# Performance work log

Measured on AMD Instinct MI355X. Metric: run time of the kernel, lower is better.

## Reference

```python
import jax, jax.numpy as jnp
import numpy as np

N = 50000      # num_nodes
E = 800000     # num_edges (avg degree 16)
IC, OC = 2, 2  # in_channels, out_channels
DIN, DOUT = 128, 128
K = 3          # number of hops


def setup_inputs() -> dict:
    key = jax.random.key(0)
    k1, k2, k3, k4 = jax.random.split(key, 4)
    x = jax.random.normal(k1, (IC, N, DIN), dtype=jnp.float32)
    edge_index = jax.random.randint(k2, (2, E), 0, N, dtype=jnp.int32)
    a = np.sqrt(6.0 / (DIN + DOUT)).astype(np.float32)  # xavier_uniform bound
    W = jax.random.uniform(k3, (OC, IC, DIN, DOUT), minval=-a, maxval=a, dtype=jnp.float32)
    params = jax.random.uniform(k4, (OC, IC, K + 1), minval=0.0, maxval=0.01, dtype=jnp.float32)
    return {"x": x, "edge_index": edge_index, "W": W, "params": params}


def reference(x, edge_index, W, params):
    # x: [IC, N, DIN]; edge_index: [2, E]; W: [OC, IC, DIN, DOUT]; params: [OC, IC, K+1]
    n = x.shape[1]
    k_hops = params.shape[-1] - 1
    row, col = edge_index[0], edge_index[1]

    # normalize_adj: symmetric D^-1/2 A D^-1/2 on unit-valued edges
    deg = jax.ops.segment_sum(jnp.ones(row.shape[0], x.dtype), row, num_segments=n)
    dinv = jnp.where(deg > 0, jax.lax.rsqrt(deg), jnp.zeros_like(deg))
    val = dinv[row] * dinv[col]  # [E]

    def spmm(X):  # A_norm @ X per channel; X: [IC, N, d]
        gathered = X[:, col, :] * val[None, :, None]  # [IC, E, d]
        return jax.vmap(lambda g: jax.ops.segment_sum(g, row, num_segments=n))(gathered)

    # Hop features: H[m] = A^m x, computed once (hoisting the redundant spmm in the torch loop)
    hops = [x]
    for _ in range(k_hops):
        hops.append(spmm(hops[-1]))
    H = jnp.stack(hops)  # [K+1, IC, N, DIN]

    # out[i] = sum_j sum_m params[i,j,m] * (A^m x_j) @ W[i,j]
    return jnp.einsum('mjnd,ijm,ijdf->inf', H, params, W)  # [OC, N, DOUT]
```

## Files before the change

### kernel.cpp

```cpp
#include <hip/hip_runtime.h>
#include <hip/hip_bf16.h>
#include <stdint.h>

#define NN 50000
#define NE 800000
#define D 128
#define KH 3
#define SCAN_B ((NN + 255) / 256)
#define SLOTS 48
#define XB 6250
#define SCB8 391
#define WBB 1024

typedef __attribute__((ext_vector_type(8))) __bf16 bf16x8;
typedef __attribute__((ext_vector_type(4))) float f32x4;
typedef uint32_t u32x2 __attribute__((ext_vector_type(2)));

__device__ __forceinline__ uint16_t bf16_rne(float f) {
  uint32_t u = __builtin_bit_cast(uint32_t, f);
  u = (u + 0x7fffu + ((u >> 16) & 1u)) >> 16;
  return (uint16_t)u;
}
__device__ __forceinline__ uint32_t bf16_pack(float lo, float hi) {
  return ((uint32_t)bf16_rne(hi) << 16) | (uint32_t)bf16_rne(lo);
}

#define GLDS16(gp, lp)                                                         \
  __builtin_amdgcn_global_load_lds(                                            \
      (__attribute__((address_space(1))) void*)(gp),                           \
      (__attribute__((address_space(3))) void*)(lp), 16, 0, 0)

__global__ void k_build3(const int* __restrict__ ei, const float* __restrict__ x,
                         const float* __restrict__ W, const float* __restrict__ params,
                         int* __restrict__ cnt, uint16_t* __restrict__ slots,
                         uint16_t* __restrict__ hop0g, uint16_t* __restrict__ wb) {
  int b = blockIdx.x, t = threadIdx.x;
  if (b < SCB8) {
    int e0 = b * 2048 + t;
    int r8[8], c8[8], p8[8];
#pragma unroll
    for (int u = 0; u < 8; ++u) {
      int e = e0 + u * 256;
      bool ok = e < NE;
      r8[u] = ok ? ei[e] : 0;
      c8[u] = ok ? ei[e + NE] : 0;
    }
#pragma unroll
    for (int u = 0; u < 8; ++u) {
      int e = e0 + u * 256;
      p8[u] = (e < NE) ? atomicAdd(&cnt[r8[u]], 1) : SLOTS;
    }
#pragma unroll
    for (int u = 0; u < 8; ++u)
      if (p8[u] < SLOTS) slots[r8[u] * SLOTS + p8[u]] = (uint16_t)c8[u];
  } else if (b < SCB8 + XB) {
    int base = ((b - SCB8) * 256 + t) * 8;
    int n = base >> 8, c0 = base & 255;
    int j = c0 >> 7, dd = c0 & 127;
    const float* xp = x + (size_t)j * NN * D + (size_t)n * D + dd;
    float4 f0 = *(const float4*)xp;
    float4 f1 = *(const float4*)(xp + 4);
    uint4 o;
    o.x = bf16_pack(f0.x, f0.y);
    o.y = bf16_pack(f0.z, f0.w);
    o.z = bf16_pack(f1.x, f1.y);
    o.w = bf16_pack(f1.z, f1.w);
    *(uint4*)(hop0g + base) = o;
  } else {
    int idx = (b - SCB8 - XB) * 256 + t;
    int c = idx >> 10, k = idx & 1023;
    int i = c >> 7, f = c & 127, m = k >> 8, j = (k >> 7) & 1, dd = k & 127;
    float p = params[(i * 2 + j) * 4 + m];
    float w = W[((i * 2 + j) * 128 + dd) * 128 + f];
    wb[idx] = bf16_rne(p * w);
  }
}

template <int P1>
__global__ void k_spmmu4(const int* __restrict__ cnt, float* __restrict__ dinvw,
                         const uint16_t* __restrict__ slots,
                         const uint16_t* __restrict__ src, uint16_t* __restrict__ dst) {
  const int lane = threadIdx.x & 63;
  const int wid = threadIdx.x >> 6;
  const int r = blockIdx.x * 4 + wid;
  if (r >= NN) return;
  const int dg = __builtin_amdgcn_readfirstlane(cnt[r]);
  const int dgc = dg < SLOTS ? dg : SLOTS;
  const int s = r * SLOTS;
  const int e = s + dgc;
  const int lo = lane * 4;

  float a0 = 0.f, a1 = 0.f, a2 = 0.f, a3 = 0.f;
  for (int i = s; i < e; i += 8) {
    int cw[8];
    float vw[8];
    u32x2 g[8];
#pragma unroll
    for (int u = 0; u < 8; ++u) {
      int idx = i + u;
      bool ok = idx < e;
      cw[u] = (int)slots[ok ? idx : e - 1];
      float vv;
      if (P1) {
        int dc = cnt[cw[u]];
        vv = (dc > 0) ? rsqrtf((float)dc) : 0.0f;
      } else {
        vv = dinvw[cw[u]];
      }
      vw[u] = ok ? vv : 0.0f;
    }
#pragma unroll
    for (int u = 0; u < 8; ++u)
      g[u] = *(const u32x2*)(src + (size_t)cw[u] * 256 + lo);
#pragma unroll
    for (int u = 0; u < 8; ++u) {
      float v = vw[u];
      a0 = fmaf(v, __builtin_bit_cast(float, g[u][0] << 16), a0);
      a1 = fmaf(v, __builtin_bit_cast(float, g[u][0] & 0xffff0000u), a1);
      a2 = fmaf(v, __builtin_bit_cast(float, g[u][1] << 16), a2);
      a3 = fmaf(v, __builtin_bit_cast(float, g[u][1] & 0xffff0000u), a3);
    }
  }
  float sc = (dg > 0) ? rsqrtf((float)dg) : 0.0f;
  if (P1 && lane == 0) dinvw[r] = sc;
  u32x2 o;
  o[0] = bf16_pack(a0 * sc, a1 * sc);
  o[1] = bf16_pack(a2 * sc, a3 * sc);
  *(u32x2*)(dst + (size_t)r * 256 + lo) = o;
}

__global__ __launch_bounds__(256) void k_gemm2(
    const uint16_t* __restrict__ h0, const uint16_t* __restrict__ h1,
    const uint16_t* __restrict__ h2, const uint16_t* __restrict__ h3,
    const uint16_t* __restrict__ wb, float* __restrict__ out) {
  __shared__ __align__(16) uint16_t As[64 * 64];
  __shared__ __align__(16) uint16_t Bs[256 * 64];
  const uint16_t* hops[4] = {h0, h1, h2, h3};
  int t = threadIdx.x;
  int lane = t & 63, wid = t >> 6;
  int wn = wid;
  int m0 = blockIdx.x * 64;
  int rl = lane & 15, q = lane >> 4;
  f32x4 acc[4][4] = {};
#pragma unroll
  for (int hop = 0; hop < 4; ++hop) {
    const uint16_t* hm = hops[hop];
#pragma unroll
    for (int kin = 0; kin < 256; kin += 64) {
      int k0 = hop * 256 + kin;
      {
#pragma unroll
        for (int rr = 0; rr < 2; ++rr) {
          int c = rr * 256 + t;
          int row = c >> 3, kcL = c & 7;
          int kcG = kcL ^ (row & 7);
          int gr = m0 + row;
          gr = gr < NN ? gr : NN - 1;
          GLDS16(hm + (size_t)gr * 256 + kin + kcG * 8, &As[c * 8]);
        }
      }
      {
#pragma unroll
        for (int rr = 0; rr < 8; ++rr) {
          int c = rr * 256 + t;
          int cc = c >> 3, kcL = c & 7;
          int kcG = kcL ^ (cc & 7);
          GLDS16(wb + (size_t)cc * 1024 + k0 + kcG * 8, &Bs[c * 8]);
        }
      }
      __syncthreads();
#pragma unroll
      for (int kq2 = 0; kq2 < 2; ++kq2) {
        int w = kq2 * 4 + q;
        bf16x8 af[4], bq[4];
#pragma unroll
        for (int f = 0; f < 4; ++f) {
          int row = f * 16 + rl;
          af[f] = *(const bf16x8*)(&As[row * 64 + (w ^ (row & 7)) * 8]);
          int col = wn * 64 + f * 16 + rl;
          bq[f] = *(const bf16x8*)(&Bs[col * 64 + (w ^ (col & 7)) * 8]);
        }
#pragma unroll
        for (int fm = 0; fm < 4; ++fm)
#pragma unroll
          for (int fn = 0; fn < 4; ++fn)
            acc[fm][fn] = __builtin_amdgcn_mfma_f32_16x16x32_bf16(af[fm], bq[fn],
                                                                  acc[fm][fn], 0, 0, 0);
      }
      __syncthreads();
    }
  }
#pragma unroll
  for (int fm = 0; fm < 4; ++fm) {
#pragma unroll
    for (int r = 0; r < 4; ++r) {
      int rowg = m0 + fm * 16 + q * 4 + r;
      if (rowg >= NN) continue;
#pragma unroll
      for (int fn = 0; fn < 4; ++fn) {
        int col = wn * 64 + fn * 16 + rl;
        int iOut = col >> 7, colg = col & 127;
        out[((size_t)iOut * NN + rowg) * D + colg] = acc[fm][fn][r];
      }
    }
  }
}

__global__ void k_deg(const int* __restrict__ row, int* __restrict__ deg) {
  int e = blockIdx.x * 256 + threadIdx.x;
  if (e < NE) atomicAdd(&deg[row[e]], 1);
}

__global__ void k_dinv_bsum(const int* __restrict__ deg, float* __restrict__ dinv,
                            int* __restrict__ bsum) {
  __shared__ int s[256];
  int t = threadIdx.x;
  int i = blockIdx.x * 256 + t;
  int d = (i < NN) ? deg[i] : 0;
  if (i < NN) dinv[i] = (d > 0) ? rsqrtf((float)d) : 0.0f;
  s[t] = d;
  __syncthreads();
  for (int off = 128; off > 0; off >>= 1) {
    if (t < off) s[t] += s[t + off];
    __syncthreads();
  }
  if (t == 0) bsum[blockIdx.x] = s[0];
}

__global__ void k_rpwrite(const int* __restrict__ deg, const int* __restrict__ bsum,
                          int* __restrict__ rp, int* __restrict__ cur) {
  __shared__ int s[256];
  __shared__ int sboff;
  int t = threadIdx.x;
  int b = blockIdx.x;
  int pv = (t < b) ? bsum[t] : 0;
  s[t] = pv;
  __syncthreads();
  for (int off = 128; off > 0; off >>= 1) {
    if (t < off) s[t] += s[t + off];
    __syncthreads();
  }
  if (t == 0) sboff = s[0];
  __syncthreads();
  int i = b * 256 + t;
  int v = (i < NN) ? deg[i] : 0;
  s[t] = v;
  __syncthreads();
  for (int off = 1; off < 256; off <<= 1) {
    int u = (t >= off) ? s[t - off] : 0;
    __syncthreads();
    s[t] += u;
    __syncthreads();
  }
  if (i < NN) {
    int r = sboff + s[t] - v;
    rp[i] = r;
    cur[i] = r;
  }
  if (i == 0) rp[NN] = NE;
}

__global__ void k_scatter(const int* __restrict__ row, const int* __restrict__ col,
                          const float* __restrict__ dinv, int* __restrict__ cur,
                          int2* __restrict__ csr) {
  int e = blockIdx.x * 256 + threadIdx.x;
  if (e < NE) {
    int r = row[e], c = col[e];
    int pos = atomicAdd(&cur[r], 1);
    csr[pos] = make_int2(c, __float_as_int(dinv[r] * dinv[c]));
  }
}

__global__ void k_wbig_f(const float* __restrict__ W, const float* __restrict__ params,
                         uint16_t* __restrict__ wb) {
  int idx = blockIdx.x * 256 + threadIdx.x;
  if (idx >= 2 * 256 * 512) return;
  int j = idx >> 17, c = (idx >> 9) & 255, k = idx & 511;
  int i = c >> 7, f = c & 127, m = k >> 7, dd = k & 127;
  float p = params[(i * 2 + j) * 4 + m];
  float w = W[((i * 2 + j) * 128 + dd) * 128 + f];
  wb[idx] = bf16_rne(p * w);
}

__global__ void k_x2h_f(const float* __restrict__ xj, uint16_t* __restrict__ dst) {
  int idx = blockIdx.x * 256 + threadIdx.x;
  if (idx < NN * D) dst[idx] = bf16_rne(xj[idx]);
}

template <int NCH>
__global__ void k_spmm(const int* __restrict__ rp, const int2* __restrict__ csr,
                       const uint16_t* __restrict__ src, uint16_t* __restrict__ dst) {
  constexpr int STRIDE = NCH * 128;
  typedef uint32_t gvec __attribute__((ext_vector_type(NCH)));
  const int lane = threadIdx.x & 63;
  const int wid = threadIdx.x >> 6;
  const int r = blockIdx.x * 4 + wid;
  if (r >= NN) return;
  const int s = __builtin_amdgcn_readfirstlane(rp[r]);
  const int e = __builtin_amdgcn_readfirstlane(rp[r + 1]);
  const int lo = lane * 2 * NCH;

  float a[2 * NCH] = {};
  for (int i = s; i < e; i += 8) {
    int2 cv[8];
    gvec g[8];
#pragma unroll
    for (int u = 0; u < 8; ++u) {
      int idx = i + u;
      bool ok = idx < e;
      cv[u] = csr[ok ? idx : e - 1];
      if (!ok) cv[u].y = 0;
    }
#pragma unroll
    for (int u = 0; u < 8; ++u)
      g[u] = *(const gvec*)(src + (size_t)cv[u].x * STRIDE + lo);
#pragma unroll
    for (int u = 0; u < 8; ++u) {
      float v = __int_as_float(cv[u].y);
#pragma unroll
      for (int q = 0; q < NCH; ++q) {
        a[2 * q] = fmaf(v, __builtin_bit_cast(float, g[u][q] << 16), a[2 * q]);
        a[2 * q + 1] =
            fmaf(v, __builtin_bit_cast(float, g[u][q] & 0xffff0000u), a[2 * q + 1]);
      }
    }
  }
  gvec o;
#pragma unroll
  for (int q = 0; q < NCH; ++q) o[q] = bf16_pack(a[2 * q], a[2 * q + 1]);
  *(gvec*)(dst + (size_t)r * STRIDE + lo) = o;
}

template <int KTOT, int HOPW, int ACCUM>
__global__ __launch_bounds__(256) void k_gemm(
    const uint16_t* __restrict__ h0, const uint16_t* __restrict__ h1,
    const uint16_t* __restrict__ h2, const uint16_t* __restrict__ h3,
    const uint16_t* __restrict__ wb, float* __restrict__ out) {
  __shared__ __align__(16) uint16_t As[128 * 64];
  __shared__ __align__(16) uint16_t Bs[128 * 64];
  const uint16_t* hops[4] = {h0, h1, h2, h3};
  int t = threadIdx.x;
  int lane = t & 63, wid = t >> 6;
  int wm = wid >> 1, wn = wid & 1;
  int m0 = blockIdx.x * 128;
  int c0 = blockIdx.y * 128;
  int rl = lane & 15, q = lane >> 4;
  f32x4 acc[4][4] = {};
#pragma unroll
  for (int hop = 0; hop < KTOT / HOPW; ++hop) {
    const uint16_t* hm = hops[hop];
#pragma unroll
    for (int kin = 0; kin < HOPW; kin += 64) {
      int k0 = hop * HOPW + kin;
#pragma unroll
      for (int rr = 0; rr < 4; ++rr) {
        int c = rr * 256 + t;
        int row = c >> 3, kcL = c & 7;
        int kcG = kcL ^ (row & 7);
        int gr = m0 + row;
        gr = gr < NN ? gr : NN - 1;
        GLDS16(hm + (size_t)gr * HOPW + kin + kcG * 8, &As[c * 8]);
      }
#pragma unroll
      for (int rr = 0; rr < 4; ++rr) {
        int c = rr * 256 + t;
        int cc = c >> 3, kcL = c & 7;
        int kcG = kcL ^ (cc & 7);
        GLDS16(wb + (size_t)(c0 + cc) * KTOT + k0 + kcG * 8, &Bs[c * 8]);
      }
      __syncthreads();
#pragma unroll
      for (int kq2 = 0; kq2 < 2; ++kq2) {
        int w = kq2 * 4 + q;
        bf16x8 af[4], bq[4];
#pragma unroll
        for (int f = 0; f < 4; ++f) {
          int row = wm * 64 + f * 16 + rl;
          af[f] = *(const bf16x8*)(&As[row * 64 + (w ^ (row & 7)) * 8]);
          int col = wn * 64 + f * 16 + rl;
          bq[f] = *(const bf16x8*)(&Bs[col * 64 + (w ^ (col & 7)) * 8]);
        }
#pragma unroll
        for (int fm = 0; fm < 4; ++fm)
#pragma unroll
          for (int fn = 0; fn < 4; ++fn)
            acc[fm][fn] = __builtin_amdgcn_mfma_f32_16x16x32_bf16(af[fm], bq[fn],
                                                                  acc[fm][fn], 0, 0, 0);
      }
      __syncthreads();
    }
  }
  int iOut = blockIdx.y;
#pragma unroll
  for (int fm = 0; fm < 4; ++fm) {
#pragma unroll
    for (int r = 0; r < 4; ++r) {
      int rowg = m0 + wm * 64 + fm * 16 + q * 4 + r;
      if (rowg >= NN) continue;
      float* op = out + ((size_t)iOut * NN + rowg) * D;
#pragma unroll
      for (int fn = 0; fn < 4; ++fn) {
        int colg = wn * 64 + fn * 16 + rl;
        if (ACCUM)
          op[colg] += acc[fm][fn][r];
        else
          op[colg] = acc[fm][fn][r];
      }
    }
  }
}

extern "C" void kernel_launch(void* const* d_in, const int* in_sizes, int n_in,
                              void* d_out, int out_size, void* d_ws, size_t ws_size,
                              hipStream_t stream) {
  (void)in_sizes; (void)n_in; (void)out_size;
  const float* x = (const float*)d_in[0];
  const int* ei = (const int*)d_in[1];
  const float* W = (const float*)d_in[2];
  const float* params = (const float*)d_in[3];
  float* out = (float*)d_out;
  char* ws = (char*)d_ws;

  size_t off = 0;
  auto take = [&](size_t bytes) {
    char* p = ws + off;
    off = (off + bytes + 255) & ~(size_t)255;
    return p;
  };

  int* cnt = (int*)take((size_t)NN * 4);
  float* dinvw = (float*)take((size_t)NN * 4);
  uint16_t* slots = (uint16_t*)take((size_t)NN * SLOTS * 2);
  uint16_t* wb = (uint16_t*)take((size_t)256 * 1024 * 2);
  size_t hopC = (size_t)NN * 256 * 2;
  size_t needC = off + 4 * hopC + 1024;

  if (ws_size >= needC) {
    uint16_t* hop0g = (uint16_t*)take(hopC);
    uint16_t* h1 = (uint16_t*)take(hopC);
    uint16_t* h2 = (uint16_t*)take(hopC);
    uint16_t* h3 = (uint16_t*)take(hopC);
    (void)hipMemsetAsync(cnt, 0, (size_t)NN * 4, stream);
    k_build3<<<SCB8 + XB + WBB, 256, 0, stream>>>(ei, x, W, params, cnt, slots,
                                                  hop0g, wb);
    k_spmmu4<1><<<(NN + 3) / 4, 256, 0, stream>>>(cnt, dinvw, slots, hop0g, h1);
    k_spmmu4<0><<<(NN + 3) / 4, 256, 0, stream>>>(cnt, dinvw, slots, h1, h2);
    k_spmmu4<0><<<(NN + 3) / 4, 256, 0, stream>>>(cnt, dinvw, slots, h2, h3);
    k_gemm2<<<(NN + 63) / 64, 256, 0, stream>>>(hop0g, h1, h2, h3, wb, out);
  } else {
    off = 0;
    int* deg = (int*)take((size_t)NN * 4);
    float* dinv = (float*)take((size_t)NN * 4);
    int* rp = (int*)take((size_t)(NN + 1) * 4);
    int* cur = (int*)take((size_t)NN * 4);
    int* bsum = (int*)take(256 * 4);
    int2* csr = (int2*)take((size_t)NE * 8);
    uint16_t* wbf = (uint16_t*)take((size_t)256 * 1024 * 2);
    (void)hipMemsetAsync(deg, 0, (size_t)NN * 4, stream);
    k_deg<<<(NE + 255) / 256, 256, 0, stream>>>(ei, deg);
    k_dinv_bsum<<<SCAN_B, 256, 0, stream>>>(deg, dinv, bsum);
    k_rpwrite<<<SCAN_B, 256, 0, stream>>>(deg, bsum, rp, cur);
    k_scatter<<<(NE + 255) / 256, 256, 0, stream>>>(ei, ei + NE, dinv, cur, csr);
    size_t hopF = (size_t)NN * 128 * 2;
    uint16_t* hop[4];
    for (int m = 0; m < 4; ++m) hop[m] = (uint16_t*)take(hopF);
    k_wbig_f<<<(2 * 256 * 512 + 255) / 256, 256, 0, stream>>>(W, params, wbf);
    for (int j = 0; j < 2; ++j) {
      k_x2h_f<<<(NN * D + 255) / 256, 256, 0, stream>>>(x + (size_t)j * NN * D, hop[0]);
      for (int m = 1; m <= KH; ++m)
        k_spmm<1><<<(NN + 3) / 4, 256, 0, stream>>>(rp, csr, hop[m - 1], hop[m]);
      dim3 grid((NN + 127) / 128, 2);
      if (j == 0)
        k_gemm<512, 128, 0><<<grid, 256, 0, stream>>>(hop[0], hop[1], hop[2], hop[3],
                                                      wbf, out);
      else
        k_gemm<512, 128, 1><<<grid, 256, 0, stream>>>(hop[0], hop[1], hop[2], hop[3],
                                                      wbf + 256 * 512, out);
    }
  }
}
```

Measured before the change: 347.9 us.

## Fuse build and three SpMM passes into one cooperative persistent kernel

```diff
diff --git a/kernel.cpp b/kernel.cpp
--- a/kernel.cpp
+++ b/kernel.cpp
@@ -1,4 +1,5 @@
 #include <hip/hip_runtime.h>
+#include <hip/hip_cooperative_groups.h>
 #include <hip/hip_bf16.h>
 #include <stdint.h>
 
@@ -11,6 +12,7 @@
 #define XB 6250
 #define SCB8 391
 #define WBB 1024
+#define MEGA_G 2048
 
 typedef __attribute__((ext_vector_type(8))) __bf16 bf16x8;
 typedef __attribute__((ext_vector_type(4))) float f32x4;
@@ -29,6 +31,117 @@
   __builtin_amdgcn_global_load_lds(                                            \
       (__attribute__((address_space(1))) void*)(gp),                           \
       (__attribute__((address_space(3))) void*)(lp), 16, 0, 0)
+
+template <int P1>
+__device__ __forceinline__ void spmm_pass(int nb, int bid, int wid, int lane,
+                                          const int* __restrict__ cnt,
+                                          float* __restrict__ dinvw,
+                                          const uint16_t* __restrict__ slots,
+                                          const uint16_t* __restrict__ src,
+                                          uint16_t* __restrict__ dst) {
+  const int NG = (NN + 3) / 4;
+  for (int g = bid; g < NG; g += nb) {
+    const int r = g * 4 + wid;
+    if (r >= NN) continue;
+    const int dg = __builtin_amdgcn_readfirstlane(cnt[r]);
+    const int dgc = dg < SLOTS ? dg : SLOTS;
+    const int s = r * SLOTS;
+    const int e = s + dgc;
+    const int lo = lane * 4;
+
+    float a0 = 0.f, a1 = 0.f, a2 = 0.f, a3 = 0.f;
+    for (int i = s; i < e; i += 8) {
+      int cw[8];
+      float vw[8];
+      u32x2 g8[8];
+#pragma unroll
+      for (int u = 0; u < 8; ++u) {
+        int idx = i + u;
+        bool ok = idx < e;
+        cw[u] = (int)slots[ok ? idx : e - 1];
+        float vv;
+        if (P1) {
+          int dc = cnt[cw[u]];
+          vv = (dc > 0) ? rsqrtf((float)dc) : 0.0f;
+        } else {
+          vv = dinvw[cw[u]];
+        }
+        vw[u] = ok ? vv : 0.0f;
+      }
+#pragma unroll
+      for (int u = 0; u < 8; ++u)
+        g8[u] = *(const u32x2*)(src + (size_t)cw[u] * 256 + lo);
+#pragma unroll
+      for (int u = 0; u < 8; ++u) {
+        float v = vw[u];
+        a0 = fmaf(v, __builtin_bit_cast(float, g8[u][0] << 16), a0);
+        a1 = fmaf(v, __builtin_bit_cast(float, g8[u][0] & 0xffff0000u), a1);
+        a2 = fmaf(v, __builtin_bit_cast(float, g8[u][1] << 16), a2);
+        a3 = fmaf(v, __builtin_bit_cast(float, g8[u][1] & 0xffff0000u), a3);
+      }
+    }
+    float sc = (dg > 0) ? rsqrtf((float)dg) : 0.0f;
+    if (P1 && lane == 0) dinvw[r] = sc;
+    u32x2 o;
+    o[0] = bf16_pack(a0 * sc, a1 * sc);
+    o[1] = bf16_pack(a2 * sc, a3 * sc);
+    *(u32x2*)(dst + (size_t)r * 256 + lo) = o;
+  }
+}
+
+__global__ __launch_bounds__(256, 8) void k_mega(
+    const int* __restrict__ ei, const float* __restrict__ x,
+    const float* __restrict__ W, const float* __restrict__ params,
+    int* __restrict__ cnt, float* __restrict__ dinvw,
+    uint16_t* __restrict__ slots, uint16_t* __restrict__ hop0g,
+    uint16_t* __restrict__ wb, uint16_t* __restrict__ h1,
+    uint16_t* __restrict__ h2, uint16_t* __restrict__ h3) {
+  namespace cg = cooperative_groups;
+  cg::grid_group grid = cg::this_grid();
+  const int t = threadIdx.x;
+  const int bid = blockIdx.x;
+  const int nb = gridDim.x;
+  const int gid = bid * 256 + t;
+  const int nthr = nb * 256;
+  const int lane = t & 63, wid = t >> 6;
+
+  for (int i = gid; i < NN; i += nthr) cnt[i] = 0;
+  grid.sync();
+
+  for (int e = gid; e < NE; e += nthr) {
+    int r = ei[e], c = ei[e + NE];
+    int pos = atomicAdd(&cnt[r], 1);
+    if (pos < SLOTS) slots[r * SLOTS + pos] = (uint16_t)c;
+  }
+  for (int it = gid; it < XB * 256; it += nthr) {
+    int base = it * 8;
+    int n = base >> 8, c0 = base & 255;
+    int j = c0 >> 7, dd = c0 & 127;
+    const float* xp = x + (size_t)j * NN * D + (size_t)n * D + dd;
+    float4 f0 = *(const float4*)xp;
+    float4 f1 = *(const float4*)(xp + 4);
+    uint4 o;
+    o.x = bf16_pack(f0.x, f0.y);
+    o.y = bf16_pack(f0.z, f0.w);
+    o.z = bf16_pack(f1.x, f1.y);
+    o.w = bf16_pack(f1.z, f1.w);
+    *(uint4*)(hop0g + base) = o;
+  }
+  for (int idx = gid; idx < 256 * 1024; idx += nthr) {
+    int c = idx >> 10, k = idx & 1023;
+    int i = c >> 7, f = c & 127, m = k >> 8, j = (k >> 7) & 1, dd = k & 127;
+    float p = params[(i * 2 + j) * 4 + m];
+    float w = W[((i * 2 + j) * 128 + dd) * 128 + f];
+    wb[idx] = bf16_rne(p * w);
+  }
+  grid.sync();
+
+  spmm_pass<1>(nb, bid, wid, lane, cnt, dinvw, slots, hop0g, h1);
+  grid.sync();
+  spmm_pass<0>(nb, bid, wid, lane, cnt, dinvw, slots, h1, h2);
+  grid.sync();
+  spmm_pass<0>(nb, bid, wid, lane, cnt, dinvw, slots, h2, h3);
+}
 
 __global__ void k_build3(const int* __restrict__ ei, const float* __restrict__ x,
                          const float* __restrict__ W, const float* __restrict__ params,
@@ -80,53 +193,8 @@
 __global__ void k_spmmu4(const int* __restrict__ cnt, float* __restrict__ dinvw,
                          const uint16_t* __restrict__ slots,
                          const uint16_t* __restrict__ src, uint16_t* __restrict__ dst) {
-  const int lane = threadIdx.x & 63;
-  const int wid = threadIdx.x >> 6;
-  const int r = blockIdx.x * 4 + wid;
-  if (r >= NN) return;
-  const int dg = __builtin_amdgcn_readfirstlane(cnt[r]);
-  const int dgc = dg < SLOTS ? dg : SLOTS;
-  const int s = r * SLOTS;
-  const int e = s + dgc;
-  const int lo = lane * 4;
-
-  float a0 = 0.f, a1 = 0.f, a2 = 0.f, a3 = 0.f;
-  for (int i = s; i < e; i += 8) {
-    int cw[8];
-    float vw[8];
-    u32x2 g[8];
-#pragma unroll
-    for (int u = 0; u < 8; ++u) {
-      int idx = i + u;
-      bool ok = idx < e;
-      cw[u] = (int)slots[ok ? idx : e - 1];
-      float vv;
-      if (P1) {
-        int dc = cnt[cw[u]];
-        vv = (dc > 0) ? rsqrtf((float)dc) : 0.0f;
-      } else {
-        vv = dinvw[cw[u]];
-      }
-      vw[u] = ok ? vv : 0.0f;
-    }
-#pragma unroll
-    for (int u = 0; u < 8; ++u)
-      g[u] = *(const u32x2*)(src + (size_t)cw[u] * 256 + lo);
-#pragma unroll
-    for (int u = 0; u < 8; ++u) {
-      float v = vw[u];
-      a0 = fmaf(v, __builtin_bit_cast(float, g[u][0] << 16), a0);
-      a1 = fmaf(v, __builtin_bit_cast(float, g[u][0] & 0xffff0000u), a1);
-      a2 = fmaf(v, __builtin_bit_cast(float, g[u][1] << 16), a2);
-      a3 = fmaf(v, __builtin_bit_cast(float, g[u][1] & 0xffff0000u), a3);
-    }
-  }
-  float sc = (dg > 0) ? rsqrtf((float)dg) : 0.0f;
-  if (P1 && lane == 0) dinvw[r] = sc;
-  u32x2 o;
-  o[0] = bf16_pack(a0 * sc, a1 * sc);
-  o[1] = bf16_pack(a2 * sc, a3 * sc);
-  *(u32x2*)(dst + (size_t)r * 256 + lo) = o;
+  spmm_pass<P1>(gridDim.x, blockIdx.x, threadIdx.x >> 6, threadIdx.x & 63, cnt,
+                dinvw, slots, src, dst);
 }
 
 __global__ __launch_bounds__(256) void k_gemm2(
@@ -414,8 +482,8 @@
                               void* d_out, int out_size, void* d_ws, size_t ws_size,
                               hipStream_t stream) {
   (void)in_sizes; (void)n_in; (void)out_size;
+  const int* ei = (const int*)d_in[1];
   const float* x = (const float*)d_in[0];
-  const int* ei = (const int*)d_in[1];
   const float* W = (const float*)d_in[2];
   const float* params = (const float*)d_in[3];
   float* out = (float*)d_out;
@@ -440,12 +508,19 @@
     uint16_t* h1 = (uint16_t*)take(hopC);
     uint16_t* h2 = (uint16_t*)take(hopC);
     uint16_t* h3 = (uint16_t*)take(hopC);
-    (void)hipMemsetAsync(cnt, 0, (size_t)NN * 4, stream);
-    k_build3<<<SCB8 + XB + WBB, 256, 0, stream>>>(ei, x, W, params, cnt, slots,
-                                                  hop0g, wb);
-    k_spmmu4<1><<<(NN + 3) / 4, 256, 0, stream>>>(cnt, dinvw, slots, hop0g, h1);
-    k_spmmu4<0><<<(NN + 3) / 4, 256, 0, stream>>>(cnt, dinvw, slots, h1, h2);
-    k_spmmu4<0><<<(NN + 3) / 4, 256, 0, stream>>>(cnt, dinvw, slots, h2, h3);
+    void* args[] = {(void*)&ei,    (void*)&x,   (void*)&W,     (void*)&params,
+                    (void*)&cnt,   (void*)&dinvw, (void*)&slots, (void*)&hop0g,
+                    (void*)&wb,    (void*)&h1,  (void*)&h2,    (void*)&h3};
+    hipError_t err = hipLaunchCooperativeKernel((void*)k_mega, dim3(MEGA_G),
+                                                dim3(256), args, 0, stream);
+    if (err != hipSuccess) {
+      (void)hipMemsetAsync(cnt, 0, (size_t)NN * 4, stream);
+      k_build3<<<SCB8 + XB + WBB, 256, 0, stream>>>(ei, x, W, params, cnt,
+                                                    slots, hop0g, wb);
+      k_spmmu4<1><<<(NN + 3) / 4, 256, 0, stream>>>(cnt, dinvw, slots, hop0g, h1);
+      k_spmmu4<0><<<(NN + 3) / 4, 256, 0, stream>>>(cnt, dinvw, slots, h1, h2);
+      k_spmmu4<0><<<(NN + 3) / 4, 256, 0, stream>>>(cnt, dinvw, slots, h2, h3);
+    }
     k_gemm2<<<(NN + 63) / 64, 256, 0, stream>>>(hop0g, h1, h2, h3, wb, out);
   } else {
     off = 0;
```

New measurement: 1.297 ms. +273.0%, slower.
